# Optimization experiments

Hardware: AMD Instinct MI355X
Metric: run time of the kernel (lower is better)

## Reference

```python
import jax, jax.numpy as jnp
import numpy as np

# Module-level constants from the source
L = 6       # n_layer
NH = 6      # n_head
D = 96      # dim_emb
HS = D // NH  # head_size = 16
FF = 4 * D  # 384
DG, DO, DA = 32, 64, 16   # dim_goal, dim_obs, dim_act
T = 1024    # history_size (input_seq_size)
B = 16      # batch
STD = 0.02  # init std per _init_weights


def setup_inputs() -> dict:
    key = jax.random.key(0)
    ks = jax.random.split(key, 16)
    n = lambda k, s: jax.random.normal(k, s, dtype=jnp.float32) * STD
    return {
        "goals": jax.random.normal(ks[0], (B, 1, DG), dtype=jnp.float32),
        "obss": jax.random.normal(ks[1], (B, T, DO), dtype=jnp.float32),
        # goal_obs_embedding: Linear(DG+DO -> D), stored [in, out]
        "w_go": n(ks[2], (DG + DO, D)), "b_go": jnp.zeros((D,), jnp.float32),
        # input_position_embedding table [T, D]
        "pos_emb": n(ks[3], (T, D)),
        # per-layer, per-head Q/K/V projections (no bias): [L, NH, D, HS]
        "wq": n(ks[4], (L, NH, D, HS)),
        "wk": n(ks[5], (L, NH, D, HS)),
        "wv": n(ks[6], (L, NH, D, HS)),
        # output projection per layer: Linear(D -> D)
        "w_proj": n(ks[7], (L, D, D)), "b_proj": jnp.zeros((L, D), jnp.float32),
        # layernorms (init: weight=1, bias=0)
        "ln1_g": jnp.ones((L, D), jnp.float32), "ln1_b": jnp.zeros((L, D), jnp.float32),
        "ln2_g": jnp.ones((L, D), jnp.float32), "ln2_b": jnp.zeros((L, D), jnp.float32),
        # feedforward: Linear(D->4D), ReLU, Linear(4D->D)
        "w_ff1": n(ks[8], (L, D, FF)), "b_ff1": jnp.zeros((L, FF), jnp.float32),
        "w_ff2": n(ks[9], (L, FF, D)), "b_ff2": jnp.zeros((L, D), jnp.float32),
        # final layernorm + act_mean head
        "lnf_g": jnp.ones((D,), jnp.float32), "lnf_b": jnp.zeros((D,), jnp.float32),
        "w_act": n(ks[10], (D, DA)), "b_act": jnp.zeros((DA,), jnp.float32),
    }


def _layernorm(x, g, b):
    m = jnp.mean(x, axis=-1, keepdims=True)
    v = jnp.var(x, axis=-1, keepdims=True)
    return (x - m) * jax.lax.rsqrt(v + 1e-5) * g + b


def reference(goals, obss, w_go, b_go, pos_emb, wq, wk, wv, w_proj, b_proj,
              ln1_g, ln1_b, ln2_g, ln2_b, w_ff1, b_ff1, w_ff2, b_ff2,
              lnf_g, lnf_b, w_act, b_act):
    b, t, _ = obss.shape
    # goal_obs = cat([goals.repeat(1, H_in, 1), obss], -1) -> embed + pos
    goal_obs = jnp.concatenate([jnp.broadcast_to(goals, (b, t, DG)), obss], axis=-1)
    x = goal_obs @ w_go + b_go + pos_emb[:t]  # [B, T, D]
    mask = jnp.tril(jnp.ones((t, t), dtype=bool))  # causal tril buffer
    scale = HS ** -0.5
    for l in range(L):
        # --- multi-head causal self-attention (dropout = eval identity) ---
        xn = _layernorm(x, ln1_g[l], ln1_b[l])
        q = jnp.einsum('btd,hdk->bhtk', xn, wq[l])
        k = jnp.einsum('btd,hdk->bhtk', xn, wk[l])
        v = jnp.einsum('btd,hdk->bhtk', xn, wv[l])
        att = jnp.einsum('bhtk,bhsk->bhts', q, k) * scale  # [B, NH, T, T]
        att = jnp.where(mask, att, -jnp.inf)
        att = jax.nn.softmax(att, axis=-1)
        o = jnp.einsum('bhts,bhsk->bhtk', att, v)          # [B, NH, T, HS]
        o = o.transpose(0, 2, 1, 3).reshape(b, t, NH * HS)  # concat heads
        x = x + o @ w_proj[l] + b_proj[l]
        # --- feedforward ---
        xn = _layernorm(x, ln2_g[l], ln2_b[l])
        x = x + jax.nn.relu(xn @ w_ff1[l] + b_ff1[l]) @ w_ff2[l] + b_ff2[l]
    x = _layernorm(x, lnf_g, lnf_b)
    return x @ w_act + b_act  # act_mean, [B, T, DA]
```

## Files before the change

kernel.cpp:

```cpp
#include <hip/hip_runtime.h>
#include <math.h>

#define B_ 16
#define T_ 1024
#define D_ 96
#define L_ 6
#define NH_ 6
#define HS_ 16
#define FF_ 384

typedef _Float16 h4 __attribute__((ext_vector_type(4)));
typedef _Float16 h8 __attribute__((ext_vector_type(8)));
typedef __fp16 g2 __attribute__((ext_vector_type(2)));
typedef __fp16 g4 __attribute__((ext_vector_type(4)));
typedef float f4 __attribute__((ext_vector_type(4)));

#define MFMA16 __builtin_amdgcn_mfma_f32_16x16x16f16

#define OFF_GO   0
#define OFF_QKV  9216
#define OFF_PROJ 175104
#define OFF_FF1  230400
#define OFF_FF2  451584
#define OFF_ACT  672768
// ... 1 lines not shown

#define QSCALE 0.3606737602222409f

static __device__ __forceinline__ h4 pk4(const float* p) {
  g2 lo = __builtin_amdgcn_cvt_pkrtz(p[0], p[1]);
  g2 hi = __builtin_amdgcn_cvt_pkrtz(p[2], p[3]);
  g4 r4 = __builtin_shufflevector(lo, hi, 0, 1, 2, 3);
  return __builtin_bit_cast(h4, r4);
}

static __device__ __forceinline__ void ldpair(const _Float16* base, int blk,
                                              int lane, h4& a, h4& b) {
  h8 t = *(const h8*)(base + (size_t)blk * 512 + lane * 8);
  a = __builtin_shufflevector(t, t, 0, 1, 2, 3);
  b = __builtin_shufflevector(t, t, 4, 5, 6, 7);
}

__global__ __launch_bounds__(256) void pack_all_kernel(
    const float* __restrict__ w_go, const float* __restrict__ wq,
    const float* __restrict__ wk, const float* __restrict__ wv,
    const float* __restrict__ w_proj, const float* __restrict__ w_ff1,
    const float* __restrict__ w_ff2, const float* __restrict__ w_act,
    _Float16* __restrict__ P) {
  int i = blockIdx.x * 256 + threadIdx.x;
  if (i >= PACK_TOTAL) return;
  float v;
  if (i < OFF_QKV) {
    int o = i, nf = o / 1536, r = o % 1536, stp = r / 512, q = r & 511;
    int lane = q >> 3, h8i = q & 7, lr = lane & 15, lg = lane >> 4;
    int st = stp * 2 + (h8i >> 2), j = h8i & 3;
// ... 28 lines not shown
    int nf = r0 / 6144, r = r0 % 6144, stp = r / 512, q = r & 511;
    int lane = q >> 3, h8i = q & 7, lr = lane & 15, lg = lane >> 4;
    int st = stp * 2 + (h8i >> 2), j = h8i & 3;
    int n = nf * 16 + lr, k = st * 16 + lg * 4 + j;
    v = w_ff2[l * 36864 + k * 96 + n];
  } else {
    int o = i - OFF_ACT, stp = o / 512, q = o & 511;
    int lane = q >> 3, h8i = q & 7, lr = lane & 15, lg = lane >> 4;
    int st = stp * 2 + (h8i >> 2), j = h8i & 3;
    int k = st * 16 + lg * 4 + j;
    v = w_act[k * 16 + lr];
  }
  P[i] = (_Float16)v;
}

template <bool EMBED, bool HEAD>
__global__ __launch_bounds__(384, 1) void stage_kernel(
    const float* __restrict__ goals, const float* __restrict__ obss,
    const float* __restrict__ pos, const float* __restrict__ b_go,
    const _Float16* __restrict__ obp, const _Float16* __restrict__ Wp,
    const float* __restrict__ bp, float* __restrict__ x,
    const _Float16* __restrict__ W1, const float* __restrict__ b1,
    const _Float16* __restrict__ W2, const float* __restrict__ b2,
    const float* __restrict__ ln2g, const float* __restrict__ ln2b,
    const float* __restrict__ lntg, const float* __restrict__ lntb,
    const _Float16* __restrict__ Wtail, const float* __restrict__ btail,
    _Float16* __restrict__ qp_, _Float16* __restrict__ kp_,
    _Float16* __restrict__ vp_, float* __restrict__ out) {
  __shared__ float smemf[16128];
#define XSH(g, row, c) ((_Float16*)smemf + (size_t)(g) * 1920 + (row) * 20 + (c))
#define HSP(g, fp) ((_Float16*)smemf + ((size_t)(g) * 12 + (fp)) * 512)
#define LNS(g, w, r, i) smemf[15360 + (((g) * 6 + (w)) * 16 + (r)) * 2 + (i)]
#define XP(g) (x + ((size_t)(blockIdx.x * 4 + (g)) * 6 + cfo) * 256 + lane * 4)
  const int tid = threadIdx.x;
  const int wave = tid >> 6, lane = tid & 63;
  const int lr = lane & 15, lg = lane >> 4;
  const int row0 = blockIdx.x * 64;
  const int bidx = row0 >> 10;
  const int row0b = row0 & 1023;
  const int cfo = wave;
  const f4 zero4 = {0.f, 0.f, 0.f, 0.f};
  int tok[4], tt[4];
#pragma unroll
  for (int g = 0; g < 4; ++g) { tok[g] = row0 + g * 16 + lr; tt[g] = tok[g] & 1023; }

  f4 xc[4], x1[4];

  if constexpr (EMBED) {
    h4 ef[4][6];
#pragma unroll
    for (int st = 0; st < 2; ++st) {
      f4 s4 = *(const f4*)(goals + bidx * 32 + st * 16 + lg * 4);
      h4 e = (h4){(_Float16)s4[0], (_Float16)s4[1], (_Float16)s4[2], (_Float16)s4[3]};
#pragma unroll
      for (int g = 0; g < 4; ++g) ef[g][st] = e;
    }
#pragma unroll
    for (int g = 0; g < 4; ++g)
#pragma unroll
      for (int st = 2; st < 6; ++st) {
        f4 s4 = *(const f4*)(obss + (size_t)(bidx * 1024 + tt[g]) * 64 +
                             (st - 2) * 16 + lg * 4);
        ef[g][st] = (h4){(_Float16)s4[0], (_Float16)s4[1], (_Float16)s4[2], (_Float16)s4[3]};
      }
    h4 wf[6];
#pragma unroll
    for (int stp = 0; stp < 3; ++stp)
      ldpair(Wp, cfo * 3 + stp, lane, wf[2 * stp], wf[2 * stp + 1]);
    f4 bb = *(const f4*)(b_go + cfo * 16 + lg * 4);
#pragma unroll
    for (int g = 0; g < 4; ++g) {
      f4 a = zero4;
#pragma unroll
      for (int st = 0; st < 6; ++st) a = MFMA16(wf[st], ef[g][st], a, 0, 0, 0);
      f4 pp = *(const f4*)(pos + (size_t)tt[g] * 96 + cfo * 16 + lg * 4);
#pragma unroll
      for (int j = 0; j < 4; ++j) xc[g][j] = a[j] + bb[j] + pp[j];
      *(f4*)XP(g) = xc[g];
    }
  } else {
    h4 obf[4][6];
#pragma unroll
    for (int g = 0; g < 4; ++g)
#pragma unroll
      for (int stp = 0; stp < 3; ++stp)
        ldpair(obp, (blockIdx.x * 4 + g) * 3 + stp, lane,
               obf[g][2 * stp], obf[g][2 * stp + 1]);
    h4 wf[6];
#pragma unroll
    for (int stp = 0; stp < 3; ++stp)
      ldpair(Wp, cfo * 3 + stp, lane, wf[2 * stp], wf[2 * stp + 1]);
    f4 bb = *(const f4*)(bp + cfo * 16 + lg * 4);
#pragma unroll
    for (int g = 0; g < 4; ++g) {
      f4 a = zero4;
#pragma unroll
      for (int st = 0; st < 6; ++st) a = MFMA16(wf[st], obf[g][st], a, 0, 0, 0);
      f4 xr = *(const f4*)XP(g);
#pragma unroll
      for (int j = 0; j < 4; ++j) x1[g][j] = a[j] + bb[j] + xr[j];
    }
#pragma unroll
    for (int g = 0; g < 4; ++g) {
      float s = x1[g][0] + x1[g][1] + x1[g][2] + x1[g][3];
      float sq = x1[g][0] * x1[g][0] + x1[g][1] * x1[g][1] +
                 x1[g][2] * x1[g][2] + x1[g][3] * x1[g][3];
      s += __shfl_xor(s, 16); sq += __shfl_xor(sq, 16);
      s += __shfl_xor(s, 32); sq += __shfl_xor(sq, 32);
      if (lane < 16) { LNS(g, wave, lr, 0) = s; LNS(g, wave, lr, 1) = sq; }
    }
    __syncthreads();
    {
      f4 gg4 = *(const f4*)(ln2g + cfo * 16 + lg * 4);
      f4 b4 = *(const f4*)(ln2b + cfo * 16 + lg * 4);
#pragma unroll
      for (int g = 0; g < 4; ++g) {
        float s = 0.f, sq = 0.f;
#pragma unroll
        for (int w = 0; w < 6; ++w) { s += LNS(g, w, lr, 0); sq += LNS(g, w, lr, 1); }
        float mean = s * (1.f / 96.f);
        float rs = rsqrtf(sq * (1.f / 96.f) - mean * mean + 1e-5f);
        h4 xn;
#pragma unroll
        for (int j = 0; j < 4; ++j)
          xn[j] = (_Float16)((x1[g][j] - mean) * rs * gg4[j] + b4[j]);
        *(h4*)XSH(g, cfo * 16 + lr, lg * 4) = xn;
      }
    }
    __syncthreads();
    h4 xnf[4][6];
#pragma unroll
    for (int g = 0; g < 4; ++g)
#pragma unroll
      for (int st = 0; st < 6; ++st)
        xnf[g][st] = *(const h4*)XSH(g, st * 16 + lr, lg * 4);
    __syncthreads();

#pragma unroll
    for (int p = 0; p < 2; ++p) {
      int nf0 = wave * 4 + p * 2;
      h4 wA[6], wB[6];
#pragma unroll
      for (int stp = 0; stp < 3; ++stp) {
        ldpair(W1, nf0 * 3 + stp, lane, wA[2 * stp], wA[2 * stp + 1]);
        ldpair(W1, (nf0 + 1) * 3 + stp, lane, wB[2 * stp], wB[2 * stp + 1]);
      }
      f4 bA = *(const f4*)(b1 + nf0 * 16 + lg * 4);
      f4 bB = *(const f4*)(b1 + (nf0 + 1) * 16 + lg * 4);
#pragma unroll
      for (int g = 0; g < 4; ++g) {
        f4 hA = zero4, hB = zero4;
#pragma unroll
        for (int st = 0; st < 6; ++st) {
          hA = MFMA16(wA[st], xnf[g][st], hA, 0, 0, 0);
          hB = MFMA16(wB[st], xnf[g][st], hB, 0, 0, 0);
        }
        h4 lo, hi;
#pragma unroll
        for (int j = 0; j < 4; ++j) {
          lo[j] = (_Float16)fmaxf(hA[j] + bA[j], 0.f);
          hi[j] = (_Float16)fmaxf(hB[j] + bB[j], 0.f);
        }
        h8 comb = __builtin_shufflevector(lo, hi, 0, 1, 2, 3, 4, 5, 6, 7);
        *(h8*)(HSP(g, wave * 2 + p) + lane * 8) = comb;
      }
    }
    h4 w2f[24];
#pragma unroll
    for (int stp = 0; stp < 12; ++stp)
      ldpair(W2, cfo * 12 + stp, lane, w2f[2 * stp], w2f[2 * stp + 1]);
    __syncthreads();
    {
      f4 b4 = *(const f4*)(b2 + cfo * 16 + lg * 4);
#pragma unroll
      for (int g = 0; g < 4; ++g) {
        f4 y = zero4;
#pragma unroll
        for (int fp = 0; fp < 12; ++fp) {
          h8 t = *(const h8*)(HSP(g, fp) + lane * 8);
          h4 lo = __builtin_shufflevector(t, t, 0, 1, 2, 3);
          h4 hi = __builtin_shufflevector(t, t, 4, 5, 6, 7);
          y = MFMA16(w2f[2 * fp], lo, y, 0, 0, 0);
          y = MFMA16(w2f[2 * fp + 1], hi, y, 0, 0, 0);
        }
#pragma unroll
        for (int j = 0; j < 4; ++j) xc[g][j] = x1[g][j] + y[j] + b4[j];
        if constexpr (!HEAD)
          *(f4*)XP(g) = xc[g];
      }
    }
  }

#pragma unroll
  for (int g = 0; g < 4; ++g) {
    float s = xc[g][0] + xc[g][1] + xc[g][2] + xc[g][3];
    float sq = xc[g][0] * xc[g][0] + xc[g][1] * xc[g][1] +
               xc[g][2] * xc[g][2] + xc[g][3] * xc[g][3];
    s += __shfl_xor(s, 16); sq += __shfl_xor(sq, 16);
    s += __shfl_xor(s, 32); sq += __shfl_xor(sq, 32);
    if (lane < 16) { LNS(g, wave, lr, 0) = s; LNS(g, wave, lr, 1) = sq; }
  }
  __syncthreads();
  {
    f4 gg4 = *(const f4*)(lntg + cfo * 16 + lg * 4);
// ... 7 lines not shown
      float rs = rsqrtf(sq * (1.f / 96.f) - mean * mean + 1e-5f);
      h4 xn;
#pragma unroll
      for (int j = 0; j < 4; ++j)
        xn[j] = (_Float16)((xc[g][j] - mean) * rs * gg4[j] + b4[j]);
      *(h4*)XSH(g, cfo * 16 + lr, lg * 4) = xn;
    }
  }
  __syncthreads();
  if constexpr (HEAD) {
    if (wave == 0) {
      h4 wt[6];
#pragma unroll
      for (int stp = 0; stp < 3; ++stp)
        ldpair(Wtail, stp, lane, wt[2 * stp], wt[2 * stp + 1]);
      f4 bb = *(const f4*)(btail + lg * 4);
#pragma unroll
      for (int g = 0; g < 4; ++g) {
        f4 a = zero4;
#pragma unroll
        for (int st = 0; st < 6; ++st) {
          h4 xf = *(const h4*)XSH(g, st * 16 + lr, lg * 4);
          a = MFMA16(wt[st], xf, a, 0, 0, 0);
        }
        f4 o;
#pragma unroll
        for (int j = 0; j < 4; ++j) o[j] = a[j] + bb[j];
        *(f4*)(out + (size_t)tok[g] * 16 + lg * 4) = o;
      }
    }
  } else {
    h4 xf[4][6];
#pragma unroll
    for (int g = 0; g < 4; ++g)
#pragma unroll
      for (int st = 0; st < 6; ++st)
        xf[g][st] = *(const h4*)XSH(g, st * 16 + lr, lg * 4);
#pragma unroll
    for (int f = 0; f < 3; ++f) {
      int nf = wave * 3 + f;
      h4 wt[6];
#pragma unroll
      for (int stp = 0; stp < 3; ++stp)
        ldpair(Wtail, nf * 3 + stp, lane, wt[2 * stp], wt[2 * stp + 1]);
#pragma unroll
      for (int g = 0; g < 4; ++g) {
        int t2 = (row0b >> 5) + (g >> 1);
        f4 a = zero4;
#pragma unroll
        for (int st = 0; st < 6; ++st) a = MFMA16(wt[st], xf[g][st], a, 0, 0, 0);
        if (nf < 12) {
          int h = nf < 6 ? nf : nf - 6;
          _Float16* dst = (nf < 6 ? qp_ : kp_) +
                          ((size_t)(bidx * NH_ + h) * 32 + t2) * 512 +
                          lane * 8 + (g & 1) * 4;
          h4 hv = {(_Float16)a[0], (_Float16)a[1], (_Float16)a[2], (_Float16)a[3]};
          *(h4*)dst = hv;
        } else {
          int hb = nf - 12;
          _Float16* vbase = vp_ + ((size_t)(bidx * NH_ + hb) * 32 + t2) * 512;
          int jb = (lr & 3) + (g & 1) * 4;
          int lgp = lr >> 2;
#pragma unroll
          for (int r = 0; r < 4; ++r)
            vbase[(lgp * 16 + lg * 4 + r) * 8 + jb] = (_Float16)a[r];
        }
      }
    }
  }
#undef XSH
#undef HSP
#undef LNS
#undef XP
}

__global__ __launch_bounds__(256, 6) void attn_mfma_kernel(
    const _Float16* __restrict__ Qp, const _Float16* __restrict__ Kp,
    const _Float16* __restrict__ Vp, _Float16* __restrict__ obp) {
  int bh = blockIdx.x;
  int wave = threadIdx.x >> 6;
  int lane = threadIdx.x & 63;
  int qb = wave * 8 + blockIdx.y;
  int lr = lane & 15;
  int lg = lane >> 4;

  const _Float16* qB = Qp + (size_t)bh * 16384;
  const _Float16* kB = Kp + (size_t)bh * 16384;
  const _Float16* vB = Vp + (size_t)bh * 16384;

  h4 qf0, qf1;
  {
    h8 t = *(const h8*)(qB + (size_t)qb * 512 + lane * 8);
    qf0 = __builtin_shufflevector(t, t, 0, 1, 2, 3);
    qf1 = __builtin_shufflevector(t, t, 4, 5, 6, 7);
  }
  f4 O0 = {0.f, 0.f, 0.f, 0.f}, O1 = {0.f, 0.f, 0.f, 0.f};
  f4 S0 = {0.f, 0.f, 0.f, 0.f}, S1 = {0.f, 0.f, 0.f, 0.f};
  const f4 zero4 = {0.f, 0.f, 0.f, 0.f};
  const h4 ones = {(_Float16)1.f, (_Float16)1.f, (_Float16)1.f, (_Float16)1.f};

  h4 kc0, kc1, vc0, vc1, kn0, kn1, vn0, vn1;
  {
    h8 kt = *(const h8*)(kB + lane * 8);
    kc0 = __builtin_shufflevector(kt, kt, 0, 1, 2, 3);
    kc1 = __builtin_shufflevector(kt, kt, 4, 5, 6, 7);
    h8 vt8 = *(const h8*)(vB + lane * 8);
    vc0 = __builtin_shufflevector(vt8, vt8, 0, 1, 2, 3);
    vc1 = __builtin_shufflevector(vt8, vt8, 4, 5, 6, 7);
  }

  for (int tt = 0; tt < qb; ++tt) {
    {
      h8 kt = *(const h8*)(kB + (size_t)(tt + 1) * 512 + lane * 8);
      kn0 = __builtin_shufflevector(kt, kt, 0, 1, 2, 3);
      kn1 = __builtin_shufflevector(kt, kt, 4, 5, 6, 7);
      h8 vt8 = *(const h8*)(vB + (size_t)(tt + 1) * 512 + lane * 8);
      vn0 = __builtin_shufflevector(vt8, vt8, 0, 1, 2, 3);
      vn1 = __builtin_shufflevector(vt8, vt8, 4, 5, 6, 7);
    }
    f4 sa0 = MFMA16(kc0, qf0, zero4, 0, 0, 0);
    f4 sa1 = MFMA16(kc1, qf0, zero4, 0, 0, 0);
    f4 sb0 = MFMA16(kc0, qf1, zero4, 0, 0, 0);
    f4 sb1 = MFMA16(kc1, qf1, zero4, 0, 0, 0);
    float pa0[4], pa1[4], pb0[4], pb1[4];
#pragma unroll
    for (int r = 0; r < 4; ++r) {
      pa0[r] = __builtin_amdgcn_exp2f(sa0[r]);
      pa1[r] = __builtin_amdgcn_exp2f(sa1[r]);
      pb0[r] = __builtin_amdgcn_exp2f(sb0[r]);
      pb1[r] = __builtin_amdgcn_exp2f(sb1[r]);
    }
    h4 fa0 = pk4(pa0), fa1 = pk4(pa1), fb0 = pk4(pb0), fb1 = pk4(pb1);
    O0 = MFMA16(fa0, vc0, O0, 0, 0, 0);
    O0 = MFMA16(fa1, vc1, O0, 0, 0, 0);
    S0 = MFMA16(fa0, ones, S0, 0, 0, 0);
    S0 = MFMA16(fa1, ones, S0, 0, 0, 0);
    O1 = MFMA16(fb0, vc0, O1, 0, 0, 0);
    O1 = MFMA16(fb1, vc1, O1, 0, 0, 0);
    S1 = MFMA16(fb0, ones, S1, 0, 0, 0);
    S1 = MFMA16(fb1, ones, S1, 0, 0, 0);
    kc0 = kn0; kc1 = kn1; vc0 = vn0; vc1 = vn1;
  }

  {
    f4 sa0 = MFMA16(kc0, qf0, zero4, 0, 0, 0);
    float pa0[4];
#pragma unroll
    for (int r = 0; r < 4; ++r)
      pa0[r] = (lg * 4 + r <= lr) ? __builtin_amdgcn_exp2f(sa0[r]) : 0.f;
    h4 fa0 = pk4(pa0);
    O0 = MFMA16(fa0, vc0, O0, 0, 0, 0);
    S0 = MFMA16(fa0, ones, S0, 0, 0, 0);

    f4 sb0 = MFMA16(kc0, qf1, zero4, 0, 0, 0);
    f4 sb1 = MFMA16(kc1, qf1, zero4, 0, 0, 0);
    float pb0[4], pb1[4];
#pragma unroll
    for (int r = 0; r < 4; ++r) {
      pb0[r] = __builtin_amdgcn_exp2f(sb0[r]);
      pb1[r] = (lg * 4 + r <= lr) ? __builtin_amdgcn_exp2f(sb1[r]) : 0.f;
    }
    h4 fb0 = pk4(pb0), fb1 = pk4(pb1);
    O1 = MFMA16(fb0, vc0, O1, 0, 0, 0);
    O1 = MFMA16(fb1, vc1, O1, 0, 0, 0);
    S1 = MFMA16(fb0, ones, S1, 0, 0, 0);
    S1 = MFMA16(fb1, ones, S1, 0, 0, 0);
  }

  int b = bh / NH_, h = bh % NH_;
  int stp = h >> 1;
  int jb = (lr & 3) + (h & 1) * 4;
  int lgp = lr >> 2;
  size_t tb0 = (size_t)b * 64 + qb * 2;
#pragma unroll
  for (int r = 0; r < 4; ++r) {
    float li0 = __builtin_amdgcn_rcpf(S0[r]);
    float li1 = __builtin_amdgcn_rcpf(S1[r]);
    size_t pos = (size_t)(lgp * 16 + lg * 4 + r) * 8 + jb;
    obp[(tb0 * 3 + stp) * 512 + pos] = (_Float16)(O0[r] * li0);
    obp[((tb0 + 1) * 3 + stp) * 512 + pos] = (_Float16)(O1[r] * li1);
  }
}

extern "C" void kernel_launch(void* const* d_in, const int* in_sizes, int n_in,
                              void* d_out, int out_size, void* d_ws, size_t ws_size,
                              hipStream_t stream) {
  const float* goals   = (const float*)d_in[0];
  const float* obss    = (const float*)d_in[1];
  const float* w_go    = (const float*)d_in[2];
  const float* b_go    = (const float*)d_in[3];
  const float* pos_emb = (const float*)d_in[4];
  const float* wq      = (const float*)d_in[5];
  const float* wk      = (const float*)d_in[6];
  const float* wv      = (const float*)d_in[7];
  const float* w_proj  = (const float*)d_in[8];
  const float* b_proj  = (const float*)d_in[9];
// ... 4 lines not shown
  const float* w_ff1   = (const float*)d_in[14];
  const float* b_ff1   = (const float*)d_in[15];
  const float* w_ff2   = (const float*)d_in[16];
  const float* b_ff2   = (const float*)d_in[17];
  const float* lnf_g   = (const float*)d_in[18];
  const float* lnf_b   = (const float*)d_in[19];
  const float* w_act   = (const float*)d_in[20];
  const float* b_act   = (const float*)d_in[21];
  float* out = (float*)d_out;

  const int M = B_ * T_;
  float* ws = (float*)d_ws;
  size_t off = 0;
  _Float16* P = (_Float16*)(ws + off); off += PACK_TOTAL / 2 + 64;
  float* x = ws + off; off += (size_t)M * 96;
  _Float16* obp = (_Float16*)(ws + off); off += (size_t)M * 48;
  _Float16* Qp = (_Float16*)(ws + off); off += (size_t)M * 48;
  _Float16* Kp = (_Float16*)(ws + off); off += (size_t)M * 48;
  _Float16* Vp = (_Float16*)(ws + off); off += (size_t)M * 48;

  pack_all_kernel<<<(PACK_TOTAL + 255) / 256, 256, 0, stream>>>(
      w_go, wq, wk, wv, w_proj, w_ff1, w_ff2, w_act, P);

  stage_kernel<true, false><<<M / 64, 384, 0, stream>>>(
      goals, obss, pos_emb, b_go, nullptr, P + OFF_GO, nullptr, x,
      nullptr, nullptr, nullptr, nullptr, nullptr, nullptr,
      ln1_g, ln1_b, P + OFF_QKV, nullptr, Qp, Kp, Vp, nullptr);

  for (int l = 0; l < L_; ++l) {
    attn_mfma_kernel<<<dim3(B_ * NH_, 8), 256, 0, stream>>>(Qp, Kp, Vp, obp);
    if (l < L_ - 1) {
      stage_kernel<false, false><<<M / 64, 384, 0, stream>>>(
          nullptr, nullptr, nullptr, nullptr, obp,
          P + OFF_PROJ + (size_t)l * 9216, b_proj + l * 96, x,
          P + OFF_FF1 + (size_t)l * 36864, b_ff1 + l * 384,
          P + OFF_FF2 + (size_t)l * 36864, b_ff2 + l * 96,
          ln2_g + l * 96, ln2_b + l * 96,
          ln1_g + (l + 1) * 96, ln1_b + (l + 1) * 96,
          P + OFF_QKV + (size_t)(l + 1) * 27648, nullptr, Qp, Kp, Vp, nullptr);
    } else {
      stage_kernel<false, true><<<M / 64, 384, 0, stream>>>(
          nullptr, nullptr, nullptr, nullptr, obp,
          P + OFF_PROJ + (size_t)l * 9216, b_proj + l * 96, x,
          P + OFF_FF1 + (size_t)l * 36864, b_ff1 + l * 384,
          P + OFF_FF2 + (size_t)l * 36864, b_ff2 + l * 96,
          ln2_g + l * 96, ln2_b + l * 96,
          lnf_g, lnf_b, P + OFF_ACT, b_act, nullptr, nullptr, nullptr, out);
    }
  }
}
```

Measured before the change: 210.9 us.

## Fuse causal attention into per-layer MLP kernel with balanced tile pairing

Removes the separate attention kernel and computes attention inside the layer kernel. Each block owns query tiles jj and 31-jj of one batch, so causal work is balanced across blocks, and each wave handles one head. The attention output goes through shared memory into the projection instead of through a global obp buffer. Q/K/V buffers are double-buffered because the next layer's QKV is written while other blocks still read the current one. The cost is 256 blocks of 384 threads running serial attention loops, which may reduce parallelism during the attention phase compared with the old 768-block attention grid.

```diff
diff --git a/kernel.cpp b/kernel.cpp
--- a/kernel.cpp
+++ b/kernel.cpp
@@ -39,6 +39,73 @@
   h8 t = *(const h8*)(base + (size_t)blk * 512 + lane * 8);
   a = __builtin_shufflevector(t, t, 0, 1, 2, 3);
   b = __builtin_shufflevector(t, t, 4, 5, 6, 7);
+}
+
+static __device__ __forceinline__ void ldkv(const _Float16* kB_, const _Float16* vB_,
+                                            int tile, int lane,
+                                            h4& k0, h4& k1, h4& v0, h4& v1) {
+  h8 kt = *(const h8*)(kB_ + (size_t)tile * 512 + lane * 8);
+  k0 = __builtin_shufflevector(kt, kt, 0, 1, 2, 3);
+  k1 = __builtin_shufflevector(kt, kt, 4, 5, 6, 7);
+  h8 vt = *(const h8*)(vB_ + (size_t)tile * 512 + lane * 8);
+  v0 = __builtin_shufflevector(vt, vt, 0, 1, 2, 3);
+  v1 = __builtin_shufflevector(vt, vt, 4, 5, 6, 7);
+}
+
+static __device__ __forceinline__ void astep_full(
+    const h4& kc0, const h4& kc1, const h4& vc0, const h4& vc1,
+    const h4& qf0, const h4& qf1, const h4& ones,
+    f4& O0, f4& O1, f4& S0, f4& S1) {
+  const f4 zero4 = {0.f, 0.f, 0.f, 0.f};
+  f4 sa0 = MFMA16(kc0, qf0, zero4, 0, 0, 0);
+  f4 sa1 = MFMA16(kc1, qf0, zero4, 0, 0, 0);
+  f4 sb0 = MFMA16(kc0, qf1, zero4, 0, 0, 0);
+  f4 sb1 = MFMA16(kc1, qf1, zero4, 0, 0, 0);
+  float pa0[4], pa1[4], pb0[4], pb1[4];
+#pragma unroll
+  for (int r = 0; r < 4; ++r) {
+    pa0[r] = __builtin_amdgcn_exp2f(sa0[r]);
+    pa1[r] = __builtin_amdgcn_exp2f(sa1[r]);
+    pb0[r] = __builtin_amdgcn_exp2f(sb0[r]);
+    pb1[r] = __builtin_amdgcn_exp2f(sb1[r]);
+  }
+  h4 fa0 = pk4(pa0), fa1 = pk4(pa1), fb0 = pk4(pb0), fb1 = pk4(pb1);
+  O0 = MFMA16(fa0, vc0, O0, 0, 0, 0);
+  O0 = MFMA16(fa1, vc1, O0, 0, 0, 0);
+  S0 = MFMA16(fa0, ones, S0, 0, 0, 0);
+  S0 = MFMA16(fa1, ones, S0, 0, 0, 0);
+  O1 = MFMA16(fb0, vc0, O1, 0, 0, 0);
+  O1 = MFMA16(fb1, vc1, O1, 0, 0, 0);
+  S1 = MFMA16(fb0, ones, S1, 0, 0, 0);
+  S1 = MFMA16(fb1, ones, S1, 0, 0, 0);
+}
+
+static __device__ __forceinline__ void astep_diag(
+    const h4& kc0, const h4& kc1, const h4& vc0, const h4& vc1,
+    const h4& qf0, const h4& qf1, const h4& ones,
+    f4& O0, f4& O1, f4& S0, f4& S1, int lr, int lg) {
+  const f4 zero4 = {0.f, 0.f, 0.f, 0.f};
+  f4 sa0 = MFMA16(kc0, qf0, zero4, 0, 0, 0);
+  float pa0[4];
+#pragma unroll
+  for (int r = 0; r < 4; ++r)
+    pa0[r] = (lg * 4 + r <= lr) ? __builtin_amdgcn_exp2f(sa0[r]) : 0.f;
+  h4 fa0 = pk4(pa0);
+  O0 = MFMA16(fa0, vc0, O0, 0, 0, 0);
+  S0 = MFMA16(fa0, ones, S0, 0, 0, 0);
+  f4 sb0 = MFMA16(kc0, qf1, zero4, 0, 0, 0);
+  f4 sb1 = MFMA16(kc1, qf1, zero4, 0, 0, 0);
+  float pb0[4], pb1[4];
+#pragma unroll
+  for (int r = 0; r < 4; ++r) {
+    pb0[r] = __builtin_amdgcn_exp2f(sb0[r]);
+    pb1[r] = (lg * 4 + r <= lr) ? __builtin_amdgcn_exp2f(sb1[r]) : 0.f;
+  }
+  h4 fb0 = pk4(pb0), fb1 = pk4(pb1);
+  O1 = MFMA16(fb0, vc0, O1, 0, 0, 0);
+  O1 = MFMA16(fb1, vc1, O1, 0, 0, 0);
+  S1 = MFMA16(fb0, ones, S1, 0, 0, 0);
+  S1 = MFMA16(fb1, ones, S1, 0, 0, 0);
 }
 
 __global__ __launch_bounds__(256) void pack_all_kernel(
@@ -97,12 +164,138 @@
   P[i] = (_Float16)v;
 }
 
-template <bool EMBED, bool HEAD>
-__global__ __launch_bounds__(384, 1) void stage_kernel(
+
+__global__ __launch_bounds__(384, 1) void embed_kernel(
     const float* __restrict__ goals, const float* __restrict__ obss,
     const float* __restrict__ pos, const float* __restrict__ b_go,
-    const _Float16* __restrict__ obp, const _Float16* __restrict__ Wp,
-    const float* __restrict__ bp, float* __restrict__ x,
+    const _Float16* __restrict__ Wp, float* __restrict__ x,
+    const float* __restrict__ lntg, const float* __restrict__ lntb,
+    const _Float16* __restrict__ Wtail,
+    _Float16* __restrict__ qp_, _Float16* __restrict__ kp_,
+    _Float16* __restrict__ vp_) {
+  __shared__ float smemf[16128];
+#define XSH(g, row, c) ((_Float16*)smemf + (size_t)(g) * 1920 + (row) * 20 + (c))
+#define LNS(g, w, r, i) smemf[15360 + (((g) * 6 + (w)) * 16 + (r)) * 2 + (i)]
+#define XP(g) (x + ((size_t)(blockIdx.x * 4 + (g)) * 6 + cfo) * 256 + lane * 4)
+  const int tid = threadIdx.x;
+  const int wave = tid >> 6, lane = tid & 63;
+  const int lr = lane & 15, lg = lane >> 4;
+  const int b = blockIdx.x >> 4, jj = blockIdx.x & 15;
+  const int cfo = wave;
+  const f4 zero4 = {0.f, 0.f, 0.f, 0.f};
+  int mrow[4] = {2 * jj, 2 * jj + 1, 62 - 2 * jj, 63 - 2 * jj};
+  int tt_[4], t2_[4];
+#pragma unroll
+  for (int g = 0; g < 4; ++g) { tt_[g] = mrow[g] * 16 + lr; t2_[g] = (g < 2) ? jj : 31 - jj; }
+
+  f4 xc[4];
+  h4 ef[4][6];
+#pragma unroll
+  for (int st = 0; st < 2; ++st) {
+    f4 s4 = *(const f4*)(goals + b * 32 + st * 16 + lg * 4);
+    h4 e = (h4){(_Float16)s4[0], (_Float16)s4[1], (_Float16)s4[2], (_Float16)s4[3]};
+#pragma unroll
+    for (int g = 0; g < 4; ++g) ef[g][st] = e;
+  }
+#pragma unroll
+  for (int g = 0; g < 4; ++g)
+#pragma unroll
+    for (int st = 2; st < 6; ++st) {
+      f4 s4 = *(const f4*)(obss + (size_t)(b * 1024 + tt_[g]) * 64 +
+                           (st - 2) * 16 + lg * 4);
+      ef[g][st] = (h4){(_Float16)s4[0], (_Float16)s4[1], (_Float16)s4[2], (_Float16)s4[3]};
+    }
+  h4 wf[6];
+#pragma unroll
+  for (int stp = 0; stp < 3; ++stp)
+    ldpair(Wp, cfo * 3 + stp, lane, wf[2 * stp], wf[2 * stp + 1]);
+  f4 bb = *(const f4*)(b_go + cfo * 16 + lg * 4);
+#pragma unroll
+  for (int g = 0; g < 4; ++g) {
+    f4 a = zero4;
+#pragma unroll
+    for (int st = 0; st < 6; ++st) a = MFMA16(wf[st], ef[g][st], a, 0, 0, 0);
+    f4 pp = *(const f4*)(pos + (size_t)tt_[g] * 96 + cfo * 16 + lg * 4);
+#pragma unroll
+    for (int j = 0; j < 4; ++j) xc[g][j] = a[j] + bb[j] + pp[j];
+    *(f4*)XP(g) = xc[g];
+  }
+
+#pragma unroll
+  for (int g = 0; g < 4; ++g) {
+    float s = xc[g][0] + xc[g][1] + xc[g][2] + xc[g][3];
+    float sq = xc[g][0] * xc[g][0] + xc[g][1] * xc[g][1] +
+               xc[g][2] * xc[g][2] + xc[g][3] * xc[g][3];
+    s += __shfl_xor(s, 16); sq += __shfl_xor(sq, 16);
+    s += __shfl_xor(s, 32); sq += __shfl_xor(sq, 32);
+    if (lane < 16) { LNS(g, wave, lr, 0) = s; LNS(g, wave, lr, 1) = sq; }
+  }
+  __syncthreads();
+  {
+    f4 gg4 = *(const f4*)(lntg + cfo * 16 + lg * 4);
+    f4 b4 = *(const f4*)(lntb + cfo * 16 + lg * 4);
+#pragma unroll
+    for (int g = 0; g < 4; ++g) {
+      float s = 0.f, sq = 0.f;
+#pragma unroll
+      for (int w = 0; w < 6; ++w) { s += LNS(g, w, lr, 0); sq += LNS(g, w, lr, 1); }
+      float mean = s * (1.f / 96.f);
+      float rs = rsqrtf(sq * (1.f / 96.f) - mean * mean + 1e-5f);
+      h4 xn;
+#pragma unroll
+      for (int j = 0; j < 4; ++j)
+        xn[j] = (_Float16)((xc[g][j] - mean) * rs * gg4[j] + b4[j]);
+      *(h4*)XSH(g, cfo * 16 + lr, lg * 4) = xn;
+    }
+  }
+  __syncthreads();
+  h4 xf[4][6];
+#pragma unroll
+  for (int g = 0; g < 4; ++g)
+#pragma unroll
+    for (int st = 0; st < 6; ++st)
+      xf[g][st] = *(const h4*)XSH(g, st * 16 + lr, lg * 4);
+#pragma unroll
+  for (int f = 0; f < 3; ++f) {
+    int nf = wave * 3 + f;
+    h4 wt[6];
+#pragma unroll
+    for (int stp = 0; stp < 3; ++stp)
+      ldpair(Wtail, nf * 3 + stp, lane, wt[2 * stp], wt[2 * stp + 1]);
+#pragma unroll
+    for (int g = 0; g < 4; ++g) {
+      f4 a = zero4;
+#pragma unroll
+      for (int st = 0; st < 6; ++st) a = MFMA16(wt[st], xf[g][st], a, 0, 0, 0);
+      if (nf < 12) {
+        int h = nf < 6 ? nf : nf - 6;
+        _Float16* dst = (nf < 6 ? qp_ : kp_) +
+                        ((size_t)(b * NH_ + h) * 32 + t2_[g]) * 512 +
+                        lane * 8 + (g & 1) * 4;
+        h4 hv = {(_Float16)a[0], (_Float16)a[1], (_Float16)a[2], (_Float16)a[3]};
+        *(h4*)dst = hv;
+      } else {
+        int hb = nf - 12;
+        _Float16* vbase = vp_ + ((size_t)(b * NH_ + hb) * 32 + t2_[g]) * 512;
+        int jb = (lr & 3) + (g & 1) * 4;
+        int lgp = lr >> 2;
+#pragma unroll
+        for (int r = 0; r < 4; ++r)
+          vbase[(lgp * 16 + lg * 4 + r) * 8 + jb] = (_Float16)a[r];
+      }
+    }
+  }
+#undef XSH
+#undef LNS
+#undef XP
+}
+
+template <bool HEAD>
+__global__ __launch_bounds__(384, 1) void layer_kernel(
+    const _Float16* __restrict__ Qs, const _Float16* __restrict__ Ks,
+    const _Float16* __restrict__ Vs,
+    const _Float16* __restrict__ Wp, const float* __restrict__ bp,
+    float* __restrict__ x,
     const _Float16* __restrict__ W1, const float* __restrict__ b1,
     const _Float16* __restrict__ W2, const float* __restrict__ b2,
     const float* __restrict__ ln2g, const float* __restrict__ ln2b,
@@ -112,165 +305,188 @@
     _Float16* __restrict__ vp_, float* __restrict__ out) {
   __shared__ float smemf[16128];
 #define XSH(g, row, c) ((_Float16*)smemf + (size_t)(g) * 1920 + (row) * 20 + (c))
+#define OSH ((_Float16*)smemf + 7680)
 #define HSP(g, fp) ((_Float16*)smemf + ((size_t)(g) * 12 + (fp)) * 512)
 #define LNS(g, w, r, i) smemf[15360 + (((g) * 6 + (w)) * 16 + (r)) * 2 + (i)]
 #define XP(g) (x + ((size_t)(blockIdx.x * 4 + (g)) * 6 + cfo) * 256 + lane * 4)
   const int tid = threadIdx.x;
   const int wave = tid >> 6, lane = tid & 63;
   const int lr = lane & 15, lg = lane >> 4;
-  const int row0 = blockIdx.x * 64;
-  const int bidx = row0 >> 10;
-  const int row0b = row0 & 1023;
+  const int b = blockIdx.x >> 4, jj = blockIdx.x & 15;
   const int cfo = wave;
   const f4 zero4 = {0.f, 0.f, 0.f, 0.f};
-  int tok[4], tt[4];
-#pragma unroll
-  for (int g = 0; g < 4; ++g) { tok[g] = row0 + g * 16 + lr; tt[g] = tok[g] & 1023; }
+  const h4 ones = {(_Float16)1.f, (_Float16)1.f, (_Float16)1.f, (_Float16)1.f};
+  int mrow[4] = {2 * jj, 2 * jj + 1, 62 - 2 * jj, 63 - 2 * jj};
+  int tt_[4], tok_[4], t2_[4];
+#pragma unroll
+  for (int g = 0; g < 4; ++g) {
+    tt_[g] = mrow[g] * 16 + lr;
+    tok_[g] = b * 1024 + tt_[g];
+    t2_[g] = (g < 2) ? jj : 31 - jj;
+  }
+
+  {
+    const size_t bhoff = (size_t)(b * NH_ + wave) * 16384;
+    const _Float16* qB_ = Qs + bhoff;
+    const _Float16* kB_ = Ks + bhoff;
+    const _Float16* vB_ = Vs + bhoff;
+    const int qA = jj, qB2 = 31 - jj;
+    h4 qfA0, qfA1, qfB0, qfB1;
+    {
+      h8 t = *(const h8*)(qB_ + (size_t)qA * 512 + lane * 8);
+      qfA0 = __builtin_shufflevector(t, t, 0, 1, 2, 3);
+      qfA1 = __builtin_shufflevector(t, t, 4, 5, 6, 7);
+      h8 t2v = *(const h8*)(qB_ + (size_t)qB2 * 512 + lane * 8);
+      qfB0 = __builtin_shufflevector(t2v, t2v, 0, 1, 2, 3);
+      qfB1 = __builtin_shufflevector(t2v, t2v, 4, 5, 6, 7);
+    }
+    f4 OA0 = zero4, OA1 = zero4, SA0 = zero4, SA1 = zero4;
+    f4 OB0 = zero4, OB1 = zero4, SB0 = zero4, SB1 = zero4;
+    h4 kc0, kc1, vc0, vc1, kn0, kn1, vn0, vn1;
+    ldkv(kB_, vB_, 0, lane, kc0, kc1, vc0, vc1);
+    for (int t3 = 0; t3 < qA; ++t3) {
+      ldkv(kB_, vB_, t3 + 1, lane, kn0, kn1, vn0, vn1);
+      astep_full(kc0, kc1, vc0, vc1, qfA0, qfA1, ones, OA0, OA1, SA0, SA1);
+      astep_full(kc0, kc1, vc0, vc1, qfB0, qfB1, ones, OB0, OB1, SB0, SB1);
+      kc0 = kn0; kc1 = kn1; vc0 = vn0; vc1 = vn1;
+    }
+    {
+      ldkv(kB_, vB_, qA + 1, lane, kn0, kn1, vn0, vn1);
+      astep_diag(kc0, kc1, vc0, vc1, qfA0, qfA1, ones, OA0, OA1, SA0, SA1, lr, lg);
+      astep_full(kc0, kc1, vc0, vc1, qfB0, qfB1, ones, OB0, OB1, SB0, SB1);
+      kc0 = kn0; kc1 = kn1; vc0 = vn0; vc1 = vn1;
+    }
+    for (int t3 = qA + 1; t3 < qB2; ++t3) {
+      ldkv(kB_, vB_, t3 + 1, lane, kn0, kn1, vn0, vn1);
+      astep_full(kc0, kc1, vc0, vc1, qfB0, qfB1, ones, OB0, OB1, SB0, SB1);
+      kc0 = kn0; kc1 = kn1; vc0 = vn0; vc1 = vn1;
+    }
+    astep_diag(kc0, kc1, vc0, vc1, qfB0, qfB1, ones, OB0, OB1, SB0, SB1, lr, lg);
+    int stp = wave >> 1;
+    int jb = (lr & 3) + (wave & 1) * 4;
+    int lgp = lr >> 2;
+#pragma unroll
+    for (int r = 0; r < 4; ++r) {
+      int pos = (lgp * 16 + lg * 4 + r) * 8 + jb;
+      OSH[(0 * 3 + stp) * 512 + pos] = (_Float16)(OA0[r] * __builtin_amdgcn_rcpf(SA0[r]));
+      OSH[(1 * 3 + stp) * 512 + pos] = (_Float16)(OA1[r] * __builtin_amdgcn_rcpf(SA1[r]));
+      OSH[(2 * 3 + stp) * 512 + pos] = (_Float16)(OB0[r] * __builtin_amdgcn_rcpf(SB0[r]));
+      OSH[(3 * 3 + stp) * 512 + pos] = (_Float16)(OB1[r] * __builtin_amdgcn_rcpf(SB1[r]));
+    }
+  }
+  __syncthreads();
 
   f4 xc[4], x1[4];
-
-  if constexpr (EMBED) {
-    h4 ef[4][6];
-#pragma unroll
-    for (int st = 0; st < 2; ++st) {
-      f4 s4 = *(const f4*)(goals + bidx * 32 + st * 16 + lg * 4);
-      h4 e = (h4){(_Float16)s4[0], (_Float16)s4[1], (_Float16)s4[2], (_Float16)s4[3]};
-#pragma unroll
-      for (int g = 0; g < 4; ++g) ef[g][st] = e;
-    }
-#pragma unroll
-    for (int g = 0; g < 4; ++g)
-#pragma unroll
-      for (int st = 2; st < 6; ++st) {
-        f4 s4 = *(const f4*)(obss + (size_t)(bidx * 1024 + tt[g]) * 64 +
-                             (st - 2) * 16 + lg * 4);
-        ef[g][st] = (h4){(_Float16)s4[0], (_Float16)s4[1], (_Float16)s4[2], (_Float16)s4[3]};
+  h4 obf[4][6];
+#pragma unroll
+  for (int g = 0; g < 4; ++g)
+#pragma unroll
+    for (int stp = 0; stp < 3; ++stp) {
+      h8 t = *(const h8*)(OSH + ((size_t)(g * 3 + stp)) * 512 + lane * 8);
+      obf[g][2 * stp] = __builtin_shufflevector(t, t, 0, 1, 2, 3);
+      obf[g][2 * stp + 1] = __builtin_shufflevector(t, t, 4, 5, 6, 7);
+    }
+  h4 wf[6];
+#pragma unroll
+  for (int stp = 0; stp < 3; ++stp)
+    ldpair(Wp, cfo * 3 + stp, lane, wf[2 * stp], wf[2 * stp + 1]);
+  f4 bb = *(const f4*)(bp + cfo * 16 + lg * 4);
+#pragma unroll
+  for (int g = 0; g < 4; ++g) {
+    f4 a = zero4;
+#pragma unroll
+    for (int st = 0; st < 6; ++st) a = MFMA16(wf[st], obf[g][st], a, 0, 0, 0);
+    f4 xr = *(const f4*)XP(g);
+#pragma unroll
+    for (int j = 0; j < 4; ++j) x1[g][j] = a[j] + bb[j] + xr[j];
+  }
+#pragma unroll
+  for (int g = 0; g < 4; ++g) {
+    float s = x1[g][0] + x1[g][1] + x1[g][2] + x1[g][3];
+    float sq = x1[g][0] * x1[g][0] + x1[g][1] * x1[g][1] +
+               x1[g][2] * x1[g][2] + x1[g][3] * x1[g][3];
+    s += __shfl_xor(s, 16); sq += __shfl_xor(sq, 16);
+    s += __shfl_xor(s, 32); sq += __shfl_xor(sq, 32);
+    if (lane < 16) { LNS(g, wave, lr, 0) = s; LNS(g, wave, lr, 1) = sq; }
+  }
+  __syncthreads();
+  {
+    f4 gg4 = *(const f4*)(ln2g + cfo * 16 + lg * 4);
+    f4 b4 = *(const f4*)(ln2b + cfo * 16 + lg * 4);
+#pragma unroll
+    for (int g = 0; g < 4; ++g) {
+      float s = 0.f, sq = 0.f;
+#pragma unroll
+      for (int w = 0; w < 6; ++w) { s += LNS(g, w, lr, 0); sq += LNS(g, w, lr, 1); }
+      float mean = s * (1.f / 96.f);
+      float rs = rsqrtf(sq * (1.f / 96.f) - mean * mean + 1e-5f);
+      h4 xn;
+#pragma unroll
+      for (int j = 0; j < 4; ++j)
+        xn[j] = (_Float16)((x1[g][j] - mean) * rs * gg4[j] + b4[j]);
+      *(h4*)XSH(g, cfo * 16 + lr, lg * 4) = xn;
+    }
+  }
+  __syncthreads();
+  h4 xnf[4][6];
+#pragma unroll
+  for (int g = 0; g < 4; ++g)
+#pragma unroll
+    for (int st = 0; st < 6; ++st)
+      xnf[g][st] = *(const h4*)XSH(g, st * 16 + lr, lg * 4);
+  __syncthreads();
+
+#pragma unroll
+  for (int p = 0; p < 2; ++p) {
+    int nf0 = wave * 4 + p * 2;
+    h4 wA[6], wB[6];
+#pragma unroll
+    for (int stp = 0; stp < 3; ++stp) {
+      ldpair(W1, nf0 * 3 + stp, lane, wA[2 * stp], wA[2 * stp + 1]);
+      ldpair(W1, (nf0 + 1) * 3 + stp, lane, wB[2 * stp], wB[2 * stp + 1]);
+    }
+    f4 bA = *(const f4*)(b1 + nf0 * 16 + lg * 4);
+    f4 bB = *(const f4*)(b1 + (nf0 + 1) * 16 + lg * 4);
+#pragma unroll
+    for (int g = 0; g < 4; ++g) {
+      f4 hA = zero4, hB = zero4;
+#pragma unroll
+      for (int st = 0; st < 6; ++st) {
+        hA = MFMA16(wA[st], xnf[g][st], hA, 0, 0, 0);
+        hB = MFMA16(wB[st], xnf[g][st], hB, 0, 0, 0);
       }
-    h4 wf[6];
-#pragma unroll
-    for (int stp = 0; stp < 3; ++stp)
-      ldpair(Wp, cfo * 3 + stp, lane, wf[2 * stp], wf[2 * stp + 1]);
-    f4 bb = *(const f4*)(b_go + cfo * 16 + lg * 4);
+      h4 lo, hi;
+#pragma unroll
+      for (int j = 0; j < 4; ++j) {
+        lo[j] = (_Float16)fmaxf(hA[j] + bA[j], 0.f);
+        hi[j] = (_Float16)fmaxf(hB[j] + bB[j], 0.f);
+      }
+      h8 comb = __builtin_shufflevector(lo, hi, 0, 1, 2, 3, 4, 5, 6, 7);
+      *(h8*)(HSP(g, wave * 2 + p) + lane * 8) = comb;
+    }
+  }
+  h4 w2f[24];
+#pragma unroll
+  for (int stp = 0; stp < 12; ++stp)
+    ldpair(W2, cfo * 12 + stp, lane, w2f[2 * stp], w2f[2 * stp + 1]);
+  __syncthreads();
+  {
+    f4 b4 = *(const f4*)(b2 + cfo * 16 + lg * 4);
 #pragma unroll
     for (int g = 0; g < 4; ++g) {
-      f4 a = zero4;
-#pragma unroll
-      for (int st = 0; st < 6; ++st) a = MFMA16(wf[st], ef[g][st], a, 0, 0, 0);
-      f4 pp = *(const f4*)(pos + (size_t)tt[g] * 96 + cfo * 16 + lg * 4);
-#pragma unroll
-      for (int j = 0; j < 4; ++j) xc[g][j] = a[j] + bb[j] + pp[j];
-      *(f4*)XP(g) = xc[g];
-    }
-  } else {
-    h4 obf[4][6];
-#pragma unroll
-    for (int g = 0; g < 4; ++g)
-#pragma unroll
-      for (int stp = 0; stp < 3; ++stp)
-        ldpair(obp, (blockIdx.x * 4 + g) * 3 + stp, lane,
-               obf[g][2 * stp], obf[g][2 * stp + 1]);
-    h4 wf[6];
-#pragma unroll
-    for (int stp = 0; stp < 3; ++stp)
-      ldpair(Wp, cfo * 3 + stp, lane, wf[2 * stp], wf[2 * stp + 1]);
-    f4 bb = *(const f4*)(bp + cfo * 16 + lg * 4);
-#pragma unroll
-    for (int g = 0; g < 4; ++g) {
-      f4 a = zero4;
-#pragma unroll
-      for (int st = 0; st < 6; ++st) a = MFMA16(wf[st], obf[g][st], a, 0, 0, 0);
-      f4 xr = *(const f4*)XP(g);
-#pragma unroll
-      for (int j = 0; j < 4; ++j) x1[g][j] = a[j] + bb[j] + xr[j];
-    }
-#pragma unroll
-    for (int g = 0; g < 4; ++g) {
-      float s = x1[g][0] + x1[g][1] + x1[g][2] + x1[g][3];
-      float sq = x1[g][0] * x1[g][0] + x1[g][1] * x1[g][1] +
-                 x1[g][2] * x1[g][2] + x1[g][3] * x1[g][3];
-      s += __shfl_xor(s, 16); sq += __shfl_xor(sq, 16);
-      s += __shfl_xor(s, 32); sq += __shfl_xor(sq, 32);
-      if (lane < 16) { LNS(g, wave, lr, 0) = s; LNS(g, wave, lr, 1) = sq; }
-    }
-    __syncthreads();
-    {
-      f4 gg4 = *(const f4*)(ln2g + cfo * 16 + lg * 4);
-      f4 b4 = *(const f4*)(ln2b + cfo * 16 + lg * 4);
-#pragma unroll
-      for (int g = 0; g < 4; ++g) {
-        float s = 0.f, sq = 0.f;
-#pragma unroll
-        for (int w = 0; w < 6; ++w) { s += LNS(g, w, lr, 0); sq += LNS(g, w, lr, 1); }
-        float mean = s * (1.f / 96.f);
-        float rs = rsqrtf(sq * (1.f / 96.f) - mean * mean + 1e-5f);
-        h4 xn;
-#pragma unroll
-        for (int j = 0; j < 4; ++j)
-          xn[j] = (_Float16)((x1[g][j] - mean) * rs * gg4[j] + b4[j]);
-        *(h4*)XSH(g, cfo * 16 + lr, lg * 4) = xn;
+      f4 y = zero4;
+#pragma unroll
+      for (int fp = 0; fp < 12; ++fp) {
+        h8 t = *(const h8*)(HSP(g, fp) + lane * 8);
+        h4 lo = __builtin_shufflevector(t, t, 0, 1, 2, 3);
+        h4 hi = __builtin_shufflevector(t, t, 4, 5, 6, 7);
+        y = MFMA16(w2f[2 * fp], lo, y, 0, 0, 0);
+        y = MFMA16(w2f[2 * fp + 1], hi, y, 0, 0, 0);
       }
-    }
-    __syncthreads();
-    h4 xnf[4][6];
-#pragma unroll
-    for (int g = 0; g < 4; ++g)
-#pragma unroll
-      for (int st = 0; st < 6; ++st)
-        xnf[g][st] = *(const h4*)XSH(g, st * 16 + lr, lg * 4);
-    __syncthreads();
-
-#pragma unroll
-    for (int p = 0; p < 2; ++p) {
-      int nf0 = wave * 4 + p * 2;
-      h4 wA[6], wB[6];
-#pragma unroll
-      for (int stp = 0; stp < 3; ++stp) {
-        ldpair(W1, nf0 * 3 + stp, lane, wA[2 * stp], wA[2 * stp + 1]);
-        ldpair(W1, (nf0 + 1) * 3 + stp, lane, wB[2 * stp], wB[2 * stp + 1]);
-      }
-      f4 bA = *(const f4*)(b1 + nf0 * 16 + lg * 4);
-      f4 bB = *(const f4*)(b1 + (nf0 + 1) * 16 + lg * 4);
-#pragma unroll
-      for (int g = 0; g < 4; ++g) {
-        f4 hA = zero4, hB = zero4;
-#pragma unroll
-        for (int st = 0; st < 6; ++st) {
-          hA = MFMA16(wA[st], xnf[g][st], hA, 0, 0, 0);
-          hB = MFMA16(wB[st], xnf[g][st], hB, 0, 0, 0);
-        }
-        h4 lo, hi;
-#pragma unroll
-        for (int j = 0; j < 4; ++j) {
-          lo[j] = (_Float16)fmaxf(hA[j] + bA[j], 0.f);
-          hi[j] = (_Float16)fmaxf(hB[j] + bB[j], 0.f);
-        }
-        h8 comb = __builtin_shufflevector(lo, hi, 0, 1, 2, 3, 4, 5, 6, 7);
-        *(h8*)(HSP(g, wave * 2 + p) + lane * 8) = comb;
-      }
-    }
-    h4 w2f[24];
-#pragma unroll
-    for (int stp = 0; stp < 12; ++stp)
-      ldpair(W2, cfo * 12 + stp, lane, w2f[2 * stp], w2f[2 * stp + 1]);
-    __syncthreads();
-    {
-      f4 b4 = *(const f4*)(b2 + cfo * 16 + lg * 4);
-#pragma unroll
-      for (int g = 0; g < 4; ++g) {
-        f4 y = zero4;
-#pragma unroll
-        for (int fp = 0; fp < 12; ++fp) {
-          h8 t = *(const h8*)(HSP(g, fp) + lane * 8);
-          h4 lo = __builtin_shufflevector(t, t, 0, 1, 2, 3);
-          h4 hi = __builtin_shufflevector(t, t, 4, 5, 6, 7);
-          y = MFMA16(w2f[2 * fp], lo, y, 0, 0, 0);
-          y = MFMA16(w2f[2 * fp + 1], hi, y, 0, 0, 0);
-        }
-#pragma unroll
-        for (int j = 0; j < 4; ++j) xc[g][j] = x1[g][j] + y[j] + b4[j];
-        if constexpr (!HEAD)
-          *(f4*)XP(g) = xc[g];
-      }
+#pragma unroll
+      for (int j = 0; j < 4; ++j) xc[g][j] = x1[g][j] + y[j] + b4[j];
+      if constexpr (!HEAD)
+        *(f4*)XP(g) = xc[g];
     }
   }
 
@@ -308,7 +524,7 @@
 #pragma unroll
       for (int stp = 0; stp < 3; ++stp)
         ldpair(Wtail, stp, lane, wt[2 * stp], wt[2 * stp + 1]);
-      f4 bb = *(const f4*)(btail + lg * 4);
+      f4 bbt = *(const f4*)(btail + lg * 4);
 #pragma unroll
       for (int g = 0; g < 4; ++g) {
         f4 a = zero4;
@@ -319,8 +535,8 @@
         }
         f4 o;
 #pragma unroll
-        for (int j = 0; j < 4; ++j) o[j] = a[j] + bb[j];
-        *(f4*)(out + (size_t)tok[g] * 16 + lg * 4) = o;
+        for (int j = 0; j < 4; ++j) o[j] = a[j] + bbt[j];
+        *(f4*)(out + (size_t)tok_[g] * 16 + lg * 4) = o;
       }
     }
   } else {
@@ -339,20 +555,19 @@
         ldpair(Wtail, nf * 3 + stp, lane, wt[2 * stp], wt[2 * stp + 1]);
 #pragma unroll
       for (int g = 0; g < 4; ++g) {
-        int t2 = (row0b >> 5) + (g >> 1);
         f4 a = zero4;
 #pragma unroll
         for (int st = 0; st < 6; ++st) a = MFMA16(wt[st], xf[g][st], a, 0, 0, 0);
         if (nf < 12) {
           int h = nf < 6 ? nf : nf - 6;
           _Float16* dst = (nf < 6 ? qp_ : kp_) +
-                          ((size_t)(bidx * NH_ + h) * 32 + t2) * 512 +
+                          ((size_t)(b * NH_ + h) * 32 + t2_[g]) * 512 +
                           lane * 8 + (g & 1) * 4;
           h4 hv = {(_Float16)a[0], (_Float16)a[1], (_Float16)a[2], (_Float16)a[3]};
           *(h4*)dst = hv;
         } else {
           int hb = nf - 12;
-          _Float16* vbase = vp_ + ((size_t)(bidx * NH_ + hb) * 32 + t2) * 512;
+          _Float16* vbase = vp_ + ((size_t)(b * NH_ + hb) * 32 + t2_[g]) * 512;
           int jb = (lr & 3) + (g & 1) * 4;
           int lgp = lr >> 2;
 #pragma unroll
@@ -363,117 +578,10 @@
     }
   }
 #undef XSH
+#undef OSH
 #undef HSP
 #undef LNS
 #undef XP
-}
-
-__global__ __launch_bounds__(256, 6) void attn_mfma_kernel(
-    const _Float16* __restrict__ Qp, const _Float16* __restrict__ Kp,
-    const _Float16* __restrict__ Vp, _Float16* __restrict__ obp) {
-  int bh = blockIdx.x;
-  int wave = threadIdx.x >> 6;
-  int lane = threadIdx.x & 63;
-  int qb = wave * 8 + blockIdx.y;
-  int lr = lane & 15;
-  int lg = lane >> 4;
-
-  const _Float16* qB = Qp + (size_t)bh * 16384;
-  const _Float16* kB = Kp + (size_t)bh * 16384;
-  const _Float16* vB = Vp + (size_t)bh * 16384;
-
-  h4 qf0, qf1;
-  {
-    h8 t = *(const h8*)(qB + (size_t)qb * 512 + lane * 8);
-    qf0 = __builtin_shufflevector(t, t, 0, 1, 2, 3);
-    qf1 = __builtin_shufflevector(t, t, 4, 5, 6, 7);
-  }
-  f4 O0 = {0.f, 0.f, 0.f, 0.f}, O1 = {0.f, 0.f, 0.f, 0.f};
-  f4 S0 = {0.f, 0.f, 0.f, 0.f}, S1 = {0.f, 0.f, 0.f, 0.f};
-  const f4 zero4 = {0.f, 0.f, 0.f, 0.f};
-  const h4 ones = {(_Float16)1.f, (_Float16)1.f, (_Float16)1.f, (_Float16)1.f};
-
-  h4 kc0, kc1, vc0, vc1, kn0, kn1, vn0, vn1;
-  {
-    h8 kt = *(const h8*)(kB + lane * 8);
-    kc0 = __builtin_shufflevector(kt, kt, 0, 1, 2, 3);
-    kc1 = __builtin_shufflevector(kt, kt, 4, 5, 6, 7);
-    h8 vt8 = *(const h8*)(vB + lane * 8);
-    vc0 = __builtin_shufflevector(vt8, vt8, 0, 1, 2, 3);
-    vc1 = __builtin_shufflevector(vt8, vt8, 4, 5, 6, 7);
-  }
-
-  for (int tt = 0; tt < qb; ++tt) {
-    {
-      h8 kt = *(const h8*)(kB + (size_t)(tt + 1) * 512 + lane * 8);
-      kn0 = __builtin_shufflevector(kt, kt, 0, 1, 2, 3);
-      kn1 = __builtin_shufflevector(kt, kt, 4, 5, 6, 7);
-      h8 vt8 = *(const h8*)(vB + (size_t)(tt + 1) * 512 + lane * 8);
-      vn0 = __builtin_shufflevector(vt8, vt8, 0, 1, 2, 3);
-      vn1 = __builtin_shufflevector(vt8, vt8, 4, 5, 6, 7);
-    }
-    f4 sa0 = MFMA16(kc0, qf0, zero4, 0, 0, 0);
-    f4 sa1 = MFMA16(kc1, qf0, zero4, 0, 0, 0);
-    f4 sb0 = MFMA16(kc0, qf1, zero4, 0, 0, 0);
-    f4 sb1 = MFMA16(kc1, qf1, zero4, 0, 0, 0);
-    float pa0[4], pa1[4], pb0[4], pb1[4];
-#pragma unroll
-    for (int r = 0; r < 4; ++r) {
-      pa0[r] = __builtin_amdgcn_exp2f(sa0[r]);
-      pa1[r] = __builtin_amdgcn_exp2f(sa1[r]);
-      pb0[r] = __builtin_amdgcn_exp2f(sb0[r]);
-      pb1[r] = __builtin_amdgcn_exp2f(sb1[r]);
-    }
-    h4 fa0 = pk4(pa0), fa1 = pk4(pa1), fb0 = pk4(pb0), fb1 = pk4(pb1);
-    O0 = MFMA16(fa0, vc0, O0, 0, 0, 0);
-    O0 = MFMA16(fa1, vc1, O0, 0, 0, 0);
-    S0 = MFMA16(fa0, ones, S0, 0, 0, 0);
-    S0 = MFMA16(fa1, ones, S0, 0, 0, 0);
-    O1 = MFMA16(fb0, vc0, O1, 0, 0, 0);
-    O1 = MFMA16(fb1, vc1, O1, 0, 0, 0);
-    S1 = MFMA16(fb0, ones, S1, 0, 0, 0);
-    S1 = MFMA16(fb1, ones, S1, 0, 0, 0);
-    kc0 = kn0; kc1 = kn1; vc0 = vn0; vc1 = vn1;
-  }
-
-  {
-    f4 sa0 = MFMA16(kc0, qf0, zero4, 0, 0, 0);
-    float pa0[4];
-#pragma unroll
-    for (int r = 0; r < 4; ++r)
-      pa0[r] = (lg * 4 + r <= lr) ? __builtin_amdgcn_exp2f(sa0[r]) : 0.f;
-    h4 fa0 = pk4(pa0);
-    O0 = MFMA16(fa0, vc0, O0, 0, 0, 0);
-    S0 = MFMA16(fa0, ones, S0, 0, 0, 0);
-
-    f4 sb0 = MFMA16(kc0, qf1, zero4, 0, 0, 0);
-    f4 sb1 = MFMA16(kc1, qf1, zero4, 0, 0, 0);
-    float pb0[4], pb1[4];
-#pragma unroll
-    for (int r = 0; r < 4; ++r) {
-      pb0[r] = __builtin_amdgcn_exp2f(sb0[r]);
-      pb1[r] = (lg * 4 + r <= lr) ? __builtin_amdgcn_exp2f(sb1[r]) : 0.f;
-    }
-    h4 fb0 = pk4(pb0), fb1 = pk4(pb1);
-    O1 = MFMA16(fb0, vc0, O1, 0, 0, 0);
-    O1 = MFMA16(fb1, vc1, O1, 0, 0, 0);
-    S1 = MFMA16(fb0, ones, S1, 0, 0, 0);
-    S1 = MFMA16(fb1, ones, S1, 0, 0, 0);
-  }
-
-  int b = bh / NH_, h = bh % NH_;
-  int stp = h >> 1;
-  int jb = (lr & 3) + (h & 1) * 4;
-  int lgp = lr >> 2;
-  size_t tb0 = (size_t)b * 64 + qb * 2;
-#pragma unroll
-  for (int r = 0; r < 4; ++r) {
-    float li0 = __builtin_amdgcn_rcpf(S0[r]);
-    float li1 = __builtin_amdgcn_rcpf(S1[r]);
-    size_t pos = (size_t)(lgp * 16 + lg * 4 + r) * 8 + jb;
-    obp[(tb0 * 3 + stp) * 512 + pos] = (_Float16)(O0[r] * li0);
-    obp[((tb0 + 1) * 3 + stp) * 512 + pos] = (_Float16)(O1[r] * li1);
-  }
 }
 
 extern "C" void kernel_launch(void* const* d_in, const int* in_sizes, int n_in,
@@ -508,38 +616,41 @@
   size_t off = 0;
   _Float16* P = (_Float16*)(ws + off); off += PACK_TOTAL / 2 + 64;
   float* x = ws + off; off += (size_t)M * 96;
-  _Float16* obp = (_Float16*)(ws + off); off += (size_t)M * 48;
-  _Float16* Qp = (_Float16*)(ws + off); off += (size_t)M * 48;
-  _Float16* Kp = (_Float16*)(ws + off); off += (size_t)M * 48;
-  _Float16* Vp = (_Float16*)(ws + off); off += (size_t)M * 48;
+  _Float16* Qb[2]; _Float16* Kb[2]; _Float16* Vb[2];
+  for (int p = 0; p < 2; ++p) {
+    Qb[p] = (_Float16*)(ws + off); off += (size_t)M * 48;
+    Kb[p] = (_Float16*)(ws + off); off += (size_t)M * 48;
+    Vb[p] = (_Float16*)(ws + off); off += (size_t)M * 48;
+  }
 
   pack_all_kernel<<<(PACK_TOTAL + 255) / 256, 256, 0, stream>>>(
       w_go, wq, wk, wv, w_proj, w_ff1, w_ff2, w_act, P);
 
-  stage_kernel<true, false><<<M / 64, 384, 0, stream>>>(
-      goals, obss, pos_emb, b_go, nullptr, P + OFF_GO, nullptr, x,
-      nullptr, nullptr, nullptr, nullptr, nullptr, nullptr,
-      ln1_g, ln1_b, P + OFF_QKV, nullptr, Qp, Kp, Vp, nullptr);
+  embed_kernel<<<256, 384, 0, stream>>>(
+      goals, obss, pos_emb, b_go, P + OFF_GO, x, ln1_g, ln1_b,
+      P + OFF_QKV, Qb[0], Kb[0], Vb[0]);
 
   for (int l = 0; l < L_; ++l) {
-    attn_mfma_kernel<<<dim3(B_ * NH_, 8), 256, 0, stream>>>(Qp, Kp, Vp, obp);
+    int sp = l & 1, dp = (l + 1) & 1;
     if (l < L_ - 1) {
-      stage_kernel<false, false><<<M / 64, 384, 0, stream>>>(
-          nullptr, nullptr, nullptr, nullptr, obp,
+      layer_kernel<false><<<256, 384, 0, stream>>>(
+          Qb[sp], Kb[sp], Vb[sp],
           P + OFF_PROJ + (size_t)l * 9216, b_proj + l * 96, x,
           P + OFF_FF1 + (size_t)l * 36864, b_ff1 + l * 384,
           P + OFF_FF2 + (size_t)l * 36864, b_ff2 + l * 96,
           ln2_g + l * 96, ln2_b + l * 96,
           ln1_g + (l + 1) * 96, ln1_b + (l + 1) * 96,
-          P + OFF_QKV + (size_t)(l + 1) * 27648, nullptr, Qp, Kp, Vp, nullptr);
+          P + OFF_QKV + (size_t)(l + 1) * 27648, nullptr,
+          Qb[dp], Kb[dp], Vb[dp], nullptr);
     } else {
-      stage_kernel<false, true><<<M / 64, 384, 0, stream>>>(
-          nullptr, nullptr, nullptr, nullptr, obp,
+      layer_kernel<true><<<256, 384, 0, stream>>>(
+          Qb[sp], Kb[sp], Vb[sp],
           P + OFF_PROJ + (size_t)l * 9216, b_proj + l * 96, x,
           P + OFF_FF1 + (size_t)l * 36864, b_ff1 + l * 384,
           P + OFF_FF2 + (size_t)l * 36864, b_ff2 + l * 96,
           ln2_g + l * 96, ln2_b + l * 96,
-          lnf_g, lnf_b, P + OFF_ACT, b_act, nullptr, nullptr, nullptr, out);
-    }
-  }
-}
+          lnf_g, lnf_b, P + OFF_ACT, b_act,
+          nullptr, nullptr, nullptr, out);
+    }
+  }
+}
```

After: 186.3 us, median of 2. 11.7% less time.
